# Kernel tuning notes

Measured on AMD Instinct MI355X. Metric: run time of the kernel, lower is better.

Reference implementation:

```python
import jax, jax.numpy as jnp
import numpy as np

N_ATOMS = 512
N_FEATURES = 64
BATCH = 8
BINS = 64
SEG_LEN = 1
LEAKY_SLOPE = 0.01


def _segments(n, length=1):
    # all pairs of segments (i,i+length),(j,j+length), i<j, excluding end1==start2
    n_seg = n - length
    i, j = np.triu_indices(n_seg, k=1)
    seg = np.stack([i, i + length, j, j + length], axis=1)
    return seg[seg[:, 1] != seg[:, 2]].astype(np.int32)


def _nnorm(v):
    return v / jnp.linalg.norm(v, axis=-1, keepdims=True)


def _writhe(segments, xyz):
    # segments: (P,4) int, xyz: (B,N,3) -> (B,P)
    smat = xyz[:, segments]                                  # (B,P,4,3)
    B, P = smat.shape[0], smat.shape[1]
    # displacements r02,r03,r12,r13 (point a in seg1 -> point b in seg2)
    disp = _nnorm((smat[:, :, None, 2:, :] - smat[:, :, :2, None, :]).reshape(B, P, 4, 3))
    idx_a = jnp.array([0, 1, 3, 2])
    idx_b = jnp.array([1, 3, 2, 0])
    crosses = _nnorm(jnp.cross(disp[:, :, idx_a], disp[:, :, idx_b]))
    dots = jnp.clip(jnp.sum(crosses * crosses[:, :, idx_b], axis=-1), -1.0, 1.0)
    omega = jnp.arcsin(dots).sum(-1)                         # (B,P)
    signs = jnp.sign(jnp.sum(
        jnp.cross(_nnorm(smat[:, :, 3] - smat[:, :, 2]), _nnorm(smat[:, :, 1] - smat[:, :, 0]))
        * disp[:, :, 0], axis=-1))
    return omega * signs / (2.0 * jnp.pi)


def _rbf(x, start=-1.0, end=1.0, number=BINS):
    # soft_one_hot_linspace, basis='gaussian', cutoff=False
    values = jnp.linspace(start, end, number, dtype=x.dtype)
    step = values[1] - values[0]
    diff = (x[..., None] - values) / step
    return jnp.exp(-(diff ** 2)) / 1.12


def setup_inputs() -> dict:
    key = jax.random.key(0)
    k = jax.random.split(key, 4)
    seg = jnp.asarray(_segments(N_ATOMS, SEG_LEN))           # (129795,4)
    return {
        "x": jax.random.normal(k[0], (BATCH, N_ATOMS, N_FEATURES), jnp.float32),
        "xyz": jax.random.normal(k[1], (BATCH, N_ATOMS, 3), jnp.float32) * 3.0,
        "segments": seg,
        "W1": jax.random.normal(k[2], (BINS, N_FEATURES), jnp.float32) / np.sqrt(BINS),
        "b1": jnp.zeros((N_FEATURES,), jnp.float32),
        "W2": jax.random.normal(k[3], (N_FEATURES, N_FEATURES), jnp.float32) / np.sqrt(N_FEATURES),
        "b2": jnp.zeros((N_FEATURES,), jnp.float32),
    }


def reference(x, xyz, segments, W1, b1, W2, b2):
    wr = _writhe(segments, xyz)                              # (B,P)
    # bidirectional edges between segment start points
    src = jnp.concatenate([segments[:, 0], segments[:, 2]])  # (E,)
    dst = jnp.concatenate([segments[:, 2], segments[:, 0]])  # (E,)
    wr_e = jnp.concatenate([wr, wr], axis=1)                 # (B,E)
    h = jax.nn.leaky_relu(_rbf(wr_e) @ W1 + b1, LEAKY_SLOPE) # (B,E,F)
    msg = (h @ W2 + b2) * x[:, src]                          # (B,E,F)
    agg = jax.vmap(lambda m: jax.ops.segment_sum(m, dst, num_segments=N_ATOMS))(msg)
    return x + agg                                           # residual update (B,N,F)
```

## Files before the change

kernel.cpp:

```cpp
#include <hip/hip_runtime.h>
#include <hip/hip_bf16.h>
#include <math.h>
#include <stdint.h>

#define N_ATOMS 512
#define NF 64
#define NB 8
#define NBINS 64
#define NSEG 511
#define NTF 8192
#define NSENT 2554
#define ETILES2 254

__device__ __forceinline__ float dot3(float ax, float ay, float az,
                                      float bx, float by, float bz) {
    return fmaf(ax, bx, fmaf(ay, by, az * bz));
}

__device__ __forceinline__ uint16_t bf16_bits(float f) {
    union { __hip_bfloat16 h; uint16_t u; } cv;
    cv.h = __float2bfloat16(f);
    return cv.u;
}

__device__ __forceinline__ float compute_wr(const float* pb, int i, int j) {
    float p0x = pb[3*i+0], p0y = pb[3*i+1], p0z = pb[3*i+2];
    float p1x = pb[3*i+3], p1y = pb[3*i+4], p1z = pb[3*i+5];
    float p2x = pb[3*j+0], p2y = pb[3*j+1], p2z = pb[3*j+2];
    float p3x = pb[3*j+3], p3y = pb[3*j+4], p3z = pb[3*j+5];

    float d0x = p2x-p0x, d0y = p2y-p0y, d0z = p2z-p0z;
    float d1x = p3x-p0x, d1y = p3y-p0y, d1z = p3z-p0z;
    float d2x = p2x-p1x, d2y = p2y-p1y, d2z = p2z-p1z;
    float d3x = p3x-p1x, d3y = p3y-p1y, d3z = p3z-p1z;
    {
        float n0 = rsqrtf(dot3(d0x,d0y,d0z,d0x,d0y,d0z)); d0x*=n0; d0y*=n0; d0z*=n0;
        float n1 = rsqrtf(dot3(d1x,d1y,d1z,d1x,d1y,d1z)); d1x*=n1; d1y*=n1; d1z*=n1;
        float n2 = rsqrtf(dot3(d2x,d2y,d2z,d2x,d2y,d2z)); d2x*=n2; d2y*=n2; d2z*=n2;
        float n3 = rsqrtf(dot3(d3x,d3y,d3z,d3x,d3y,d3z)); d3x*=n3; d3y*=n3; d3z*=n3;
    }
    float c0x = d0y*d1z - d0z*d1y, c0y = d0z*d1x - d0x*d1z, c0z = d0x*d1y - d0y*d1x;
    float c1x = d1y*d3z - d1z*d3y, c1y = d1z*d3x - d1x*d3z, c1z = d1x*d3y - d1y*d3x;
    float c3x = d2y*d0z - d2z*d0y, c3y = d2z*d0x - d2x*d0z, c3z = d2x*d0y - d2y*d0x;
    {
        float n0 = rsqrtf(dot3(c0x,c0y,c0z,c0x,c0y,c0z)); c0x*=n0; c0y*=n0; c0z*=n0;
        float n1 = rsqrtf(dot3(c1x,c1y,c1z,c1x,c1y,c1z)); c1x*=n1; c1y*=n1; c1z*=n1;
        float n3 = rsqrtf(dot3(c3x,c3y,c3z,c3x,c3y,c3z)); c3x*=n3; c3y*=n3; c3z*=n3;
    }
    float t0 = fminf(fmaxf(dot3(c0x,c0y,c0z, c1x,c1y,c1z), -1.f), 1.f);
    float t1 = fminf(fmaxf(dot3(c1x,c1y,c1z, c3x,c3y,c3z), -1.f), 1.f);
    float t3 = fminf(fmaxf(dot3(c3x,c3y,c3z, c0x,c0y,c0z), -1.f), 1.f);
    float omega = asinf(t0) + asinf(t1) + asinf(t3) + 1.5707963267948966f;
    float ex = p3x-p2x, ey = p3y-p2y, ez = p3z-p2z;
    float fx = p1x-p0x, fy = p1y-p0y, fz = p1z-p0z;
    float gx = ey*fz - ez*fy, gy = ez*fx - ex*fz, gz = ex*fy - ey*fx;
    float sgd = dot3(gx,gy,gz, d0x,d0y,d0z);
    float sgn = (sgd > 0.f) ? 1.f : ((sgd < 0.f) ? -1.f : 0.f);
    return omega * sgn * 0.15915494309189535f;
}

__device__ __forceinline__ uint32_t wr_to_off(float w) {
    float tf = (w + 1.0f) * ((float)(NTF - 1) * 0.5f);
    tf = fminf(fmaxf(tf, 0.0f), (float)(NTF - 1));
    int t0 = (int)(tf + 0.5f);
    t0 = (t0 > NTF - 1) ? (NTF - 1) : t0;
    return (uint32_t)t0 << 6;
}

__launch_bounds__(256)
__global__ void prepass(
        const float* __restrict__ xyz, const int* __restrict__ seg,
        const float* __restrict__ x, float* __restrict__ out,
        const float* __restrict__ W1, const float* __restrict__ b1,
        const float* __restrict__ W2, const float* __restrict__ b2,
        uint16_t* __restrict__ tabh, uint32_t* __restrict__ ta, int P) {
    __shared__ float lds[1536];

    const unsigned bx = blockIdx.x;

    if (bx < NTF / 8) {
        const int widx = threadIdx.x >> 6;
        const int lane = threadIdx.x & 63;
        const int g = bx * 4 + widx;
        const int g2 = g + NTF / 2;

        float tta = ((-1.0f + (2.0f / (float)(NTF - 1)) * (float)g)  + 1.0f) * 31.5f;
        float ttb = ((-1.0f + (2.0f / (float)(NTF - 1)) * (float)g2) + 1.0f) * 31.5f;

        float a0=0.f,a1=0.f,a2=0.f,a3=0.f, e0=0.f,e1=0.f,e2=0.f,e3=0.f;
        #pragma unroll
        for (int k = 0; k < NBINS; k += 4) {
            #pragma unroll
            for (int q = 0; q < 4; ++q) {
                float da = tta - (float)(k + q);
                float db = ttb - (float)(k + q);
                float ra = __expf(-da * da) * 0.8928571428571429f;
                float rb = __expf(-db * db) * 0.8928571428571429f;
                float wv = W1[(k + q) * NF + lane];
                if (q == 0) { a0 = fmaf(ra, wv, a0); e0 = fmaf(rb, wv, e0); }
                if (q == 1) { a1 = fmaf(ra, wv, a1); e1 = fmaf(rb, wv, e1); }
                if (q == 2) { a2 = fmaf(ra, wv, a2); e2 = fmaf(rb, wv, e2); }
                if (q == 3) { a3 = fmaf(ra, wv, a3); e3 = fmaf(rb, wv, e3); }
            }
        }
        float ha = ((a0 + a1) + (a2 + a3)) + b1[lane];
        float hb = ((e0 + e1) + (e2 + e3)) + b1[lane];
        ha = fmaxf(ha, 0.01f * ha);
        hb = fmaxf(hb, 0.01f * hb);
        lds[widx * 64 + lane]       = ha;
        lds[256 + widx * 64 + lane] = hb;
        __syncthreads();

        float m0=0.f,m1=0.f,m2=0.f,m3=0.f, n0=0.f,n1=0.f,n2=0.f,n3=0.f;
        #pragma unroll
        for (int k = 0; k < NF; k += 4) {
            float w0 = W2[(k + 0) * NF + lane];
            float w1v = W2[(k + 1) * NF + lane];
            float w2v = W2[(k + 2) * NF + lane];
            float w3 = W2[(k + 3) * NF + lane];
            m0 = fmaf(lds[widx * 64 + k + 0], w0, m0);
            m1 = fmaf(lds[widx * 64 + k + 1], w1v, m1);
            m2 = fmaf(lds[widx * 64 + k + 2], w2v, m2);
            m3 = fmaf(lds[widx * 64 + k + 3], w3, m3);
            n0 = fmaf(lds[256 + widx * 64 + k + 0], w0, n0);
            n1 = fmaf(lds[256 + widx * 64 + k + 1], w1v, n1);
            n2 = fmaf(lds[256 + widx * 64 + k + 2], w2v, n2);
            n3 = fmaf(lds[256 + widx * 64 + k + 3], w3, n3);
        }
        float ma = ((m0 + m1) + (m2 + m3)) + b2[lane];
        float mb = ((n0 + n1) + (n2 + n3)) + b2[lane];
        tabh[g  * NF + lane] = bf16_bits(ma);
        tabh[g2 * NF + lane] = bf16_bits(mb);
        if (g == 0) tabh[NTF * NF + lane] = 0;
    } else if (bx < NTF / 8 + NB * ETILES2) {
        const int rel = bx - NTF / 8;
        const int b = rel / ETILES2;
        const int tile = rel - b * ETILES2;

        const float* xb = xyz + b * (N_ATOMS * 3);
        #pragma unroll
        for (int k = 0; k < 6; ++k)
            lds[k * 256 + threadIdx.x] = xb[k * 256 + threadIdx.x];
        __syncthreads();

        #pragma unroll
        for (int q = 0; q < 2; ++q) {
            const int e = tile * 512 + q * 256 + threadIdx.x;
            if (e < P) {
                int4 sv = ((const int4*)seg)[e];
                const int i = sv.x;
                const int j = sv.z;
                uint32_t u = wr_to_off(compute_wr(lds, i, j));
                ta[(b << 18) + (i << 9) + j] = u;
                ta[(b << 18) + (j << 9) + i] = u;
            }
        }
    } else if (bx < NTF / 8 + NB * ETILES2 + 1024) {
        const int tid = (bx - (NTF / 8 + NB * ETILES2)) * 256 + threadIdx.x;
        out[tid] = x[tid];
    } else {
        const int idx = (bx - (NTF / 8 + NB * ETILES2 + 1024)) * 256 + threadIdx.x;
        if (idx < NB * NSENT) {
            const int b = idx / NSENT;
            const int k = idx - b * NSENT;
            int d, s;
            if      (k < 512)  { d = k;        s = k;     }
            else if (k < 1023) { d = k - 512;  s = d + 1; }
            else if (k < 1534) { s = k - 1023; d = s + 1; }
            else if (k < 2044) { d = k - 1534; s = NSEG;  }
            else               { s = k - 2044; d = NSEG;  }
            ta[(b << 18) + (d << 9) + s] = (uint32_t)NTF << 6;
        }
    }
}

__launch_bounds__(1024)
__global__ void agg10(
        const float* __restrict__ x, const uint32_t* __restrict__ ta,
        const uint16_t* __restrict__ tabh, float* __restrict__ out) {
    __shared__ float lds_x[4096];

    const int widx = threadIdx.x >> 6;
    const int lane = threadIdx.x & 63;
    const int bid = blockIdx.x;
    const int c    = bid & 7;
    const int dgrp = (bid >> 3) & 31;
    const int b    = bid >> 8;
    const int dst  = dgrp * 16 + widx;

    const float* xc = x + ((size_t)b << 15) + (c << 12);
    #pragma unroll
    for (int k = 0; k < 4; ++k)
        lds_x[k * 1024 + threadIdx.x] = xc[k * 1024 + threadIdx.x];
    __syncthreads();

    if (dst < NSEG) {
        const int tav = (int)ta[((size_t)b << 18) + (dst << 9) + (c << 6) + lane];

        float acc = 0.0f;
        #pragma unroll
        for (int ee = 0; ee < 64; ++ee) {
            const int off = __builtin_amdgcn_readlane(tav, ee);
            const float mv = __uint_as_float((uint32_t)tabh[off + lane] << 16);
            acc = fmaf(mv, lds_x[(ee << 6) + lane], acc);
        }
        atomicAdd(&out[((size_t)b << 15) + (dst << 6) + lane], acc);
    }
}


__global__ void init_out_kernel(const float* __restrict__ x, float* __restrict__ out, int n) {
    int idx = blockIdx.x * blockDim.x + threadIdx.x;
    if (idx < n) out[idx] = x[idx];
}

__device__ __forceinline__ void compute_m(
        const float* __restrict__ pb, int i, int j,
        const float* __restrict__ W1, const float* __restrict__ b1,
        const float* __restrict__ W2, const float* __restrict__ b2,
        float* __restrict__ mout) {
    float wr = compute_wr(pb, i, j);
    float acc_[NBINS];
    {
        float tt = (wr + 1.0f) * 31.5f;
        #pragma unroll
        for (int k = 0; k < NBINS; ++k) {
            float d = tt - (float)k;
            acc_[k] = __expf(-d * d) * 0.8928571428571429f;
        }
    }
    float h_[NF];
    #pragma unroll
    for (int f = 0; f < NF; ++f) h_[f] = b1[f];
    #pragma unroll
    for (int k = 0; k < NBINS; ++k) {
        float r = acc_[k];
        #pragma unroll
        for (int f = 0; f < NF; ++f) h_[f] = fmaf(r, W1[k * NF + f], h_[f]);
    }
    #pragma unroll
    for (int f = 0; f < NF; ++f) h_[f] = fmaxf(h_[f], 0.01f * h_[f]);
    #pragma unroll
    for (int f = 0; f < NF; ++f) acc_[f] = b2[f];
    #pragma unroll
    for (int k = 0; k < NF; ++k) {
        float hk = h_[k];
        #pragma unroll
        for (int f = 0; f < NF; ++f) acc_[f] = fmaf(hk, W2[k * NF + f], acc_[f]);
    }
    #pragma unroll
    for (int f = 0; f < NF; ++f) mout[f] = acc_[f];
}

__launch_bounds__(256, 2)
__global__ void writhe_msg_atomic_kernel(
        const float* __restrict__ x, const float* __restrict__ xyz,
        const int* __restrict__ seg,
        const float* __restrict__ W1, const float* __restrict__ b1,
        const float* __restrict__ W2, const float* __restrict__ b2,
        float* __restrict__ out, int P, int n_tiles) {
    __shared__ __hip_bfloat16 lds_m[4][64 * 65];
    __shared__ int lds_i[4][64];
    __shared__ int lds_j[4][64];

    const int widx = threadIdx.x >> 6;
    const int lane = threadIdx.x & 63;
    const int wave_g = blockIdx.x * 4 + widx;
    const int b = wave_g / n_tiles;
    const int tile = wave_g - b * n_tiles;
    const int bc = (b < NB) ? b : 0;
    const int e = tile * 64 + lane;
    const bool valid = (b < NB) && (e < P);

    int4 sv = valid ? ((const int4*)seg)[e] : make_int4(0, 1, 2, 3);
    const int i = sv.x;
    const int j = sv.z;

    float m[NF];
    compute_m(xyz + bc * (N_ATOMS * 3), i, j, W1, b1, W2, b2, m);

    const float scale = valid ? 1.0f : 0.0f;
    #pragma unroll
    for (int f = 0; f < NF; ++f)
        lds_m[widx][lane * 65 + f] = __float2bfloat16(m[f] * scale);
    lds_i[widx][lane] = i;
    lds_j[widx][lane] = j;
    __syncthreads();

    const float* xb = x + bc * (N_ATOMS * NF);
    float* ob = out + bc * (N_ATOMS * NF);
    int cur_i = lds_i[widx][0];
    float acc_i = 0.0f;
    for (int ee = 0; ee < 64; ++ee) {
        int ie = lds_i[widx][ee];
        int je = lds_j[widx][ee];
        float mv = __bfloat162float(lds_m[widx][ee * 65 + lane]);
        float xi = xb[ie * NF + lane];
        float xj = xb[je * NF + lane];
        atomicAdd(&ob[je * NF + lane], mv * xi);
        if (ie != cur_i) {
            atomicAdd(&ob[cur_i * NF + lane], acc_i);
            acc_i = 0.0f;
            cur_i = ie;
        }
        acc_i = fmaf(mv, xj, acc_i);
    }
    atomicAdd(&ob[cur_i * NF + lane], acc_i);
}

extern "C" void kernel_launch(void* const* d_in, const int* in_sizes, int n_in,
                              void* d_out, int out_size, void* d_ws, size_t ws_size,
                              hipStream_t stream) {
    const float* x   = (const float*)d_in[0];
    const float* xyz = (const float*)d_in[1];
    const int*   seg = (const int*)d_in[2];
    const float* W1  = (const float*)d_in[3];
    const float* b1  = (const float*)d_in[4];
    const float* W2  = (const float*)d_in[5];
    const float* b2  = (const float*)d_in[6];
    float* out = (float*)d_out;

    const int P = in_sizes[2] / 4;
    const int n_tiles = (P + 63) / 64;

    const size_t tabh_bytes = (size_t)(NTF + 1) * NF * sizeof(uint16_t);
    const size_t ta_bytes   = (size_t)NB * N_ATOMS * N_ATOMS * sizeof(uint32_t);
    const size_t need_ws = tabh_bytes + ta_bytes;

    if (ws_size >= need_ws && P <= ETILES2 * 512) {
        uint16_t* tabh = (uint16_t*)d_ws;
        uint32_t* ta   = (uint32_t*)((char*)d_ws + tabh_bytes);

        const int nsent_blocks = (NB * NSENT + 255) / 256;
        const int total_blocks = NTF / 8 + NB * ETILES2 + 1024 + nsent_blocks;
        hipLaunchKernelGGL(prepass, dim3(total_blocks), dim3(256), 0, stream,
                           xyz, seg, x, out, W1, b1, W2, b2, tabh, ta, P);

        hipLaunchKernelGGL(agg10, dim3(NB * 32 * 8), dim3(1024), 0, stream,
                           x, ta, tabh, out);
    } else {
        const int n = out_size;
        hipLaunchKernelGGL(init_out_kernel, dim3((n + 255) / 256), dim3(256), 0, stream,
                           x, out, n);
        const int total_waves = NB * n_tiles;
        const int blocks = (total_waves + 3) / 4;
        hipLaunchKernelGGL(writhe_msg_atomic_kernel, dim3(blocks), dim3(256), 0, stream,
                           x, xyz, seg, W1, b1, W2, b2, out, P, n_tiles);
    }
}
```

Before: 110.7 us.

## Aggregate all source chunks per block with double-buffered LDS and no atomics

The aggregation kernel is restructured so that each block owns 8 destination atoms and loops over all 8 source chunks itself. The x tile for the next chunk is double-buffered in LDS while the current one is used. The residual is added and the result stored with a plain write, instead of atomically adding partial sums into an output that the prepass had pre-initialised with a copy of x. This removes the prepass copy blocks and the global atomics. In exchange the grid is much smaller, 512 blocks of 512 threads instead of 2048 blocks of 1024, and each wave runs a serial chain of table gathers eight times longer, which reduces the parallelism available to hide latency.

```diff
diff --git a/kernel.cpp b/kernel.cpp
--- a/kernel.cpp
+++ b/kernel.cpp
@@ -70,7 +70,6 @@
 __launch_bounds__(256)
 __global__ void prepass(
         const float* __restrict__ xyz, const int* __restrict__ seg,
-        const float* __restrict__ x, float* __restrict__ out,
         const float* __restrict__ W1, const float* __restrict__ b1,
         const float* __restrict__ W2, const float* __restrict__ b2,
         uint16_t* __restrict__ tabh, uint32_t* __restrict__ ta, int P) {
@@ -155,11 +154,8 @@
                 ta[(b << 18) + (j << 9) + i] = u;
             }
         }
-    } else if (bx < NTF / 8 + NB * ETILES2 + 1024) {
-        const int tid = (bx - (NTF / 8 + NB * ETILES2)) * 256 + threadIdx.x;
-        out[tid] = x[tid];
     } else {
-        const int idx = (bx - (NTF / 8 + NB * ETILES2 + 1024)) * 256 + threadIdx.x;
+        const int idx = (bx - (NTF / 8 + NB * ETILES2)) * 256 + threadIdx.x;
         if (idx < NB * NSENT) {
             const int b = idx / NSENT;
             const int k = idx - b * NSENT;
@@ -174,38 +170,49 @@
     }
 }
 
-__launch_bounds__(1024)
-__global__ void agg10(
+__launch_bounds__(512)
+__global__ void agg11(
         const float* __restrict__ x, const uint32_t* __restrict__ ta,
         const uint16_t* __restrict__ tabh, float* __restrict__ out) {
-    __shared__ float lds_x[4096];
+    __shared__ float xs[8192];
 
     const int widx = threadIdx.x >> 6;
     const int lane = threadIdx.x & 63;
-    const int bid = blockIdx.x;
-    const int c    = bid & 7;
-    const int dgrp = (bid >> 3) & 31;
-    const int b    = bid >> 8;
-    const int dst  = dgrp * 16 + widx;
-
-    const float* xc = x + ((size_t)b << 15) + (c << 12);
-    #pragma unroll
-    for (int k = 0; k < 4; ++k)
-        lds_x[k * 1024 + threadIdx.x] = xc[k * 1024 + threadIdx.x];
-    __syncthreads();
-
-    if (dst < NSEG) {
-        const int tav = (int)ta[((size_t)b << 18) + (dst << 9) + (c << 6) + lane];
-
-        float acc = 0.0f;
+    const int bid  = blockIdx.x;
+    const int b    = bid >> 6;
+    const int dst  = ((bid & 63) << 3) + widx;
+
+    const float* xb = x + ((size_t)b << 15);
+    const uint32_t* tarow = ta + ((size_t)b << 18) + ((size_t)dst << 9);
+
+    #pragma unroll
+    for (int k = 0; k < 8; ++k)
+        xs[k * 512 + threadIdx.x] = xb[k * 512 + threadIdx.x];
+
+    float acc = 0.0f;
+    for (int c = 0; c < 8; ++c) {
+        const int tavc = (int)tarow[(c << 6) + lane];
+
+        __syncthreads();
+
+        if (c < 7) {
+            const float* xsrc = xb + ((c + 1) << 12);
+            float* xdst = xs + (((c + 1) & 1) << 12);
+            #pragma unroll
+            for (int k = 0; k < 8; ++k)
+                xdst[k * 512 + threadIdx.x] = xsrc[k * 512 + threadIdx.x];
+        }
+
+        const float* xc = xs + ((c & 1) << 12) + lane;
         #pragma unroll
         for (int ee = 0; ee < 64; ++ee) {
-            const int off = __builtin_amdgcn_readlane(tav, ee);
+            const int off = __builtin_amdgcn_readlane(tavc, ee);
             const float mv = __uint_as_float((uint32_t)tabh[off + lane] << 16);
-            acc = fmaf(mv, lds_x[(ee << 6) + lane], acc);
-        }
-        atomicAdd(&out[((size_t)b << 15) + (dst << 6) + lane], acc);
-    }
+            acc = fmaf(mv, xc[ee << 6], acc);
+        }
+    }
+
+    out[((size_t)b << 15) + (dst << 6) + lane] = xb[(dst << 6) + lane] + acc;
 }
 
 
@@ -332,11 +339,11 @@
         uint32_t* ta   = (uint32_t*)((char*)d_ws + tabh_bytes);
 
         const int nsent_blocks = (NB * NSENT + 255) / 256;
-        const int total_blocks = NTF / 8 + NB * ETILES2 + 1024 + nsent_blocks;
+        const int total_blocks = NTF / 8 + NB * ETILES2 + nsent_blocks;
         hipLaunchKernelGGL(prepass, dim3(total_blocks), dim3(256), 0, stream,
-                           xyz, seg, x, out, W1, b1, W2, b2, tabh, ta, P);
-
-        hipLaunchKernelGGL(agg10, dim3(NB * 32 * 8), dim3(1024), 0, stream,
+                           xyz, seg, W1, b1, W2, b2, tabh, ta, P);
+
+        hipLaunchKernelGGL(agg11, dim3(NB * 64), dim3(512), 0, stream,
                            x, ta, tabh, out);
     } else {
         const int n = out_size;
```

Result: slower. 117.6 us (+6.2%).
